# Optimization experiments

Hardware: AMD Instinct MI355X
Metric: run time of the kernel (lower is better)

The kernel has to match this reference:

```python
import jax, jax.numpy as jnp
import numpy as np

B = 262144      # batch of states (PPO rollout)
J = 16          # num_pools -> state_dim=32, action_dim=256
M = 12          # num_epochs_per_day (experts)
H = 34          # hidden_dim (fixed in source)
A = J * J


def setup_inputs() -> dict:
    key = jax.random.key(0)
    ks = jax.random.split(key, 6)
    states = jax.random.normal(ks[0], (B, 2 * J), dtype=jnp.float32)
    epoch_idx = jax.random.randint(ks[1], (B,), 0, M, dtype=jnp.int32)
    # fc1: kaiming normal (relu), zero bias
    W1 = jax.random.normal(ks[2], (H, 2 * J), dtype=jnp.float32) * np.sqrt(2.0 / (2 * J))
    b1 = jnp.zeros((H,), dtype=jnp.float32)
    # m expert output layers [M, A, H]
    Wout = jax.random.normal(ks[3], (M, A, H), dtype=jnp.float32) * np.sqrt(1.0 / H)
    bout = jax.random.normal(ks[4], (M, A), dtype=jnp.float32) * np.sqrt(1.0 / H)
    mask = jax.random.randint(ks[5], (J, J), 0, 2, dtype=jnp.int32)
    return {"states": states, "epoch_idx": epoch_idx, "W1": W1, "b1": b1,
            "Wout": Wout, "bout": bout, "mask": mask}


def reference(states, epoch_idx, W1, b1, Wout, bout, mask):
    # shared trunk: [B, H]
    x = jax.nn.relu(jnp.einsum('bs,hs->bh', states, W1) + b1)
    # grouped expert GEMM via one-hot routing (equivalent to output_layers[epoch_idx])
    onehot = jax.nn.one_hot(epoch_idx, M, dtype=x.dtype)           # [B, M]
    xe = x[:, None, :] * onehot[:, :, None]                        # [B, M, H]
    logits = jnp.einsum('bmh,mah->ba', xe, Wout) + bout[epoch_idx]  # [B, A]
    logits = logits.reshape(-1, J, J)
    NEG = jnp.float32(-1e9)
    return jnp.where(mask == 0, NEG, logits)
```

## Files before the change

### kernel.cpp

```cpp
#include <hip/hip_runtime.h>

typedef __attribute__((ext_vector_type(8))) short short8;
typedef __attribute__((ext_vector_type(4))) float f32x4;
typedef __attribute__((ext_vector_type(4))) int   i32x4;

#define SDIM 32
#define HDIM 34
#define NEXP 12
#define ACOL 256
#define SPB  256
#define MAXROWS 432
#define STG_STRIDE 260

__device__ __forceinline__ unsigned int bpack(float lo, float hi) {
    unsigned int a = __builtin_bit_cast(unsigned int, lo);
    unsigned int b = __builtin_bit_cast(unsigned int, hi);
    return ((a + 0x8000u) >> 16) | ((b + 0x8000u) & 0xffff0000u);
}

__global__ __launch_bounds__(256) void actor_kernel(
    const float* __restrict__ states,
    const int*   __restrict__ epoch_idx,
    const float* __restrict__ W1,
    const float* __restrict__ b1,
    const float* __restrict__ Wout,
    const float* __restrict__ bout,
    const int*   __restrict__ mask,
    float*       __restrict__ out,
    int nB)
{
    __shared__ unsigned int xs[MAXROWS * 32];
    __shared__ float stg[16 * STG_STRIDE];
    __shared__ unsigned short rowid[MAXROWS];
    __shared__ float w1s[HDIM * SDIM];
    __shared__ float b1s[HDIM];
    __shared__ int   cnt[NEXP];
    __shared__ int   goff[NEXP];
    __shared__ int   ntl[NEXP];

    const int t  = threadIdx.x;
    const int s0 = blockIdx.x * SPB;

    for (int i = t; i < HDIM * SDIM; i += 256) w1s[i] = W1[i];
    if (t < HDIM) b1s[t] = b1[t];
    if (t < NEXP) cnt[t] = 0;
    {
        f32x4 z = {0.f, 0.f, 0.f, 0.f};
        f32x4* xz = (f32x4*)xs;
        for (int i = t; i < MAXROWS * 8; i += 256) xz[i] = z;
        for (int i = t; i < MAXROWS; i += 256) rowid[i] = 0xFFFFu;
    }
    const int  sidx  = s0 + t;
    const bool valid = (sidx < nB);
    int e = 0, rank = 0;
    float sr[SDIM];
    if (valid) {
        const float4* sp = (const float4*)(states + (size_t)sidx * SDIM);
        #pragma unroll
        for (int q = 0; q < SDIM / 4; ++q) {
            float4 v = sp[q];
            sr[4*q+0] = v.x; sr[4*q+1] = v.y; sr[4*q+2] = v.z; sr[4*q+3] = v.w;
        }
        e = epoch_idx[sidx];
        rank = atomicAdd(&cnt[e], 1);
    }
    __syncthreads();

    if (t == 0) {
        int base = 0;
        #pragma unroll
        for (int i = 0; i < NEXP; ++i) {
            goff[i] = base;
            int nt = (cnt[i] + 15) >> 4;
            ntl[i] = nt;
            base += nt << 4;
        }
    }
    float x[HDIM];
    if (valid) {
        #pragma unroll 2
        for (int h = 0; h < HDIM; ++h) {
            float acc = b1s[h];
            const float4* wr = (const float4*)(w1s + h * SDIM);
            #pragma unroll
            for (int q = 0; q < SDIM / 4; ++q) {
                float4 wv = wr[q];
                acc = fmaf(sr[4*q+0], wv.x, acc);
                acc = fmaf(sr[4*q+1], wv.y, acc);
                acc = fmaf(sr[4*q+2], wv.z, acc);
                acc = fmaf(sr[4*q+3], wv.w, acc);
            }
            x[h] = fmaxf(acc, 0.0f);
        }
    }
    __syncthreads();

    if (valid) {
        const int slot = goff[e] + rank;
        const unsigned int swz = (unsigned int)((slot & 7) << 4);
        char* rbase = (char*)xs + slot * 128;
        unsigned int d[17];
        #pragma unroll
        for (int k = 0; k < 17; ++k) d[k] = bpack(x[2*k], x[2*k+1]);
        #pragma unroll
        for (int c = 0; c < 4; ++c) {
            f32x4 q;
            q[0] = __builtin_bit_cast(float, d[4*c+0]);
            q[1] = __builtin_bit_cast(float, d[4*c+1]);
            q[2] = __builtin_bit_cast(float, d[4*c+2]);
            q[3] = __builtin_bit_cast(float, d[4*c+3]);
            *(f32x4*)(rbase + ((unsigned)(c * 16) ^ swz)) = q;
        }
        *(unsigned int*)(rbase + (64u ^ swz)) = d[16];
        rowid[slot] = (unsigned short)t;
    }
    __syncthreads();

    const int wv   = t >> 6;
    const int lane = t & 63;
    const int r    = lane & 15;
    const int g    = lane >> 4;
    const int colbase = wv * 64 + r;
    const float NEG = -1e9f;
    const i32x4 mq = *(const i32x4*)(mask + 4 * lane);

    float* outb = out + (size_t)s0 * ACOL;

    for (int e2 = 0; e2 < NEXP; ++e2) {
        const int nt = ntl[e2];
        if (nt == 0) continue;

        short8 bf1[4], bf2[4];
        float  bias[4];
        #pragma unroll
        for (int j = 0; j < 4; ++j) {
            const int col = colbase + j * 16;
            const float* wr = Wout + ((size_t)e2 * ACOL + col) * HDIM;
            const float2* wp = (const float2*)(wr + g * 8);
            float2 p0 = wp[0], p1 = wp[1], p2 = wp[2], p3 = wp[3];
            uint4 q1 = make_uint4(bpack(p0.x, p0.y), bpack(p1.x, p1.y),
                                  bpack(p2.x, p2.y), bpack(p3.x, p3.y));
            bf1[j] = __builtin_bit_cast(short8, q1);
            uint4 q2 = make_uint4(0u, 0u, 0u, 0u);
            if (g == 0) q2.x = bpack(wr[32], wr[33]);
            bf2[j] = __builtin_bit_cast(short8, q2);
            bias[j] = bout[e2 * ACOL + col];
        }

        const int tb = goff[e2];
        for (int st = 0; st < nt; ++st) {
            const int rb  = tb + (st << 4);
            const int row = rb + r;
            const unsigned int swz = (unsigned int)((row & 7) << 4);
            const char* rp = (const char*)xs + row * 128;
            short8 a1 = *(const short8*)(rp + ((unsigned)(g * 16) ^ swz));
            short8 a2 = *(const short8*)(rp + ((unsigned)(64 + g * 16) ^ swz));

            f32x4 acc[4];
            #pragma unroll
            for (int j = 0; j < 4; ++j) {
                f32x4 a = {bias[j], bias[j], bias[j], bias[j]};
                a = __builtin_amdgcn_mfma_f32_16x16x32_bf16(a1, bf1[j], a, 0, 0, 0);
                a = __builtin_amdgcn_mfma_f32_16x16x32_bf16(a2, bf2[j], a, 0, 0, 0);
                acc[j] = a;
            }

            __syncthreads();
            #pragma unroll
            for (int j = 0; j < 4; ++j) {
                const int c = colbase + j * 16;
                #pragma unroll
                for (int i = 0; i < 4; ++i)
                    stg[(g * 4 + i) * STG_STRIDE + c] = acc[j][i];
            }
            __syncthreads();

            #pragma unroll
            for (int q = 0; q < 4; ++q) {
                const int lrow = wv * 4 + q;
                const unsigned rid = rowid[rb + lrow];
                f32x4 v = *(const f32x4*)&stg[lrow * STG_STRIDE + 4 * lane];
                v[0] = mq[0] ? v[0] : NEG;
                v[1] = mq[1] ? v[1] : NEG;
                v[2] = mq[2] ? v[2] : NEG;
                v[3] = mq[3] ? v[3] : NEG;
                if (rid != 0xFFFFu)
                    __builtin_nontemporal_store(v,
                        (f32x4*)(outb + (size_t)rid * ACOL + 4 * lane));
            }
        }
    }
}

extern "C" void kernel_launch(void* const* d_in, const int* in_sizes, int n_in,
                              void* d_out, int out_size, void* d_ws, size_t ws_size,
                              hipStream_t stream) {
    const float* states    = (const float*)d_in[0];
    const int*   epoch_idx = (const int*)  d_in[1];
    const float* W1        = (const float*)d_in[2];
    const float* b1        = (const float*)d_in[3];
    const float* Wout      = (const float*)d_in[4];
    const float* bout      = (const float*)d_in[5];
    const int*   mask      = (const int*)  d_in[6];
    float*       out       = (float*)d_out;

    const int nB   = in_sizes[0] / SDIM;
    const int grid = (nB + SPB - 1) / SPB;
    actor_kernel<<<grid, 256, 0, stream>>>(states, epoch_idx, W1, b1,
                                           Wout, bout, mask, out, nB);
}
```

Measured before the change: 98.36 us.

## Transpose MFMA output to store rows directly, removing LDS staging and barriers

Swaps the A/B operands of the MFMA so that each lane holds four consecutive output columns of one row. Lanes then write masked logits straight to global memory, with no LDS staging buffer and no two block barriers per tile. It also packs the trunk activations into 64-byte LDS rows, with the last pair kept in a separate array, and drops the zero-initialisation of the activation buffer. Masking becomes an fminf against a precomputed INF/-1e9 vector, and launch bounds request 4 blocks per CU. The trade-offs are that stores are no longer nontemporal and that masking via fminf changes NaN handling slightly.

```diff
diff --git a/kernel.cpp b/kernel.cpp
--- a/kernel.cpp
+++ b/kernel.cpp
@@ -10,7 +10,8 @@
 #define ACOL 256
 #define SPB  256
 #define MAXROWS 432
-#define STG_STRIDE 260
+#undef  MAXROWS
+#define MAXROWS 448
 
 __device__ __forceinline__ unsigned int bpack(float lo, float hi) {
     unsigned int a = __builtin_bit_cast(unsigned int, lo);
@@ -18,7 +19,7 @@
     return ((a + 0x8000u) >> 16) | ((b + 0x8000u) & 0xffff0000u);
 }
 
-__global__ __launch_bounds__(256) void actor_kernel(
+__global__ __launch_bounds__(256, 4) void actor_kernel(
     const float* __restrict__ states,
     const int*   __restrict__ epoch_idx,
     const float* __restrict__ W1,
@@ -29,14 +30,12 @@
     float*       __restrict__ out,
     int nB)
 {
-    __shared__ unsigned int xs[MAXROWS * 32];
-    __shared__ float stg[16 * STG_STRIDE];
+    __shared__ __align__(16) unsigned int xs[MAXROWS * 16];
+    __shared__ unsigned int   xt[MAXROWS];
     __shared__ unsigned short rowid[MAXROWS];
     __shared__ float w1s[HDIM * SDIM];
     __shared__ float b1s[HDIM];
-    __shared__ int   cnt[NEXP];
-    __shared__ int   goff[NEXP];
-    __shared__ int   ntl[NEXP];
+    __shared__ int   cnt[NEXP], goff[NEXP], ntl[NEXP];
 
     const int t  = threadIdx.x;
     const int s0 = blockIdx.x * SPB;
@@ -44,26 +43,25 @@
     for (int i = t; i < HDIM * SDIM; i += 256) w1s[i] = W1[i];
     if (t < HDIM) b1s[t] = b1[t];
     if (t < NEXP) cnt[t] = 0;
-    {
-        f32x4 z = {0.f, 0.f, 0.f, 0.f};
-        f32x4* xz = (f32x4*)xs;
-        for (int i = t; i < MAXROWS * 8; i += 256) xz[i] = z;
-        for (int i = t; i < MAXROWS; i += 256) rowid[i] = 0xFFFFu;
-    }
+    for (int i = t; i < MAXROWS; i += 256) rowid[i] = 0xFFFFu;
+
     const int  sidx  = s0 + t;
     const bool valid = (sidx < nB);
-    int e = 0, rank = 0;
     float sr[SDIM];
+    int e = 0;
     if (valid) {
-        const float4* sp = (const float4*)(states + (size_t)sidx * SDIM);
+        const f32x4* sp = (const f32x4*)(states + (size_t)sidx * SDIM);
         #pragma unroll
         for (int q = 0; q < SDIM / 4; ++q) {
-            float4 v = sp[q];
-            sr[4*q+0] = v.x; sr[4*q+1] = v.y; sr[4*q+2] = v.z; sr[4*q+3] = v.w;
+            f32x4 v = sp[q];
+            sr[4*q+0] = v[0]; sr[4*q+1] = v[1]; sr[4*q+2] = v[2]; sr[4*q+3] = v[3];
         }
         e = epoch_idx[sidx];
-        rank = atomicAdd(&cnt[e], 1);
-    }
+    }
+    __syncthreads();
+
+    int rank = 0;
+    if (valid) rank = atomicAdd(&cnt[e], 1);
     __syncthreads();
 
     if (t == 0) {
@@ -97,11 +95,11 @@
 
     if (valid) {
         const int slot = goff[e] + rank;
-        const unsigned int swz = (unsigned int)((slot & 7) << 4);
-        char* rbase = (char*)xs + slot * 128;
-        unsigned int d[17];
-        #pragma unroll
-        for (int k = 0; k < 17; ++k) d[k] = bpack(x[2*k], x[2*k+1]);
+        const unsigned swz = (unsigned)(slot & 3) << 4;
+        char* rbase = (char*)xs + slot * 64;
+        unsigned d[16];
+        #pragma unroll
+        for (int k = 0; k < 16; ++k) d[k] = bpack(x[2*k], x[2*k+1]);
         #pragma unroll
         for (int c = 0; c < 4; ++c) {
             f32x4 q;
@@ -109,9 +107,9 @@
             q[1] = __builtin_bit_cast(float, d[4*c+1]);
             q[2] = __builtin_bit_cast(float, d[4*c+2]);
             q[3] = __builtin_bit_cast(float, d[4*c+3]);
-            *(f32x4*)(rbase + ((unsigned)(c * 16) ^ swz)) = q;
-        }
-        *(unsigned int*)(rbase + (64u ^ swz)) = d[16];
+            *(f32x4*)(rbase + (((unsigned)(c * 16)) ^ swz)) = q;
+        }
+        xt[slot]    = bpack(x[32], x[33]);
         rowid[slot] = (unsigned short)t;
     }
     __syncthreads();
@@ -120,73 +118,74 @@
     const int lane = t & 63;
     const int r    = lane & 15;
     const int g    = lane >> 4;
-    const int colbase = wv * 64 + r;
+    const int cb0  = wv * 64 + 4 * g;
     const float NEG = -1e9f;
-    const i32x4 mq = *(const i32x4*)(mask + 4 * lane);
+    const float INF = __builtin_bit_cast(float, 0x7f800000u);
+
+    f32x4 mf[4];
+    #pragma unroll
+    for (int j = 0; j < 4; ++j) {
+        i32x4 mq = *(const i32x4*)(mask + cb0 + 16 * j);
+        mf[j][0] = mq[0] ? INF : NEG;
+        mf[j][1] = mq[1] ? INF : NEG;
+        mf[j][2] = mq[2] ? INF : NEG;
+        mf[j][3] = mq[3] ? INF : NEG;
+    }
 
     float* outb = out + (size_t)s0 * ACOL;
 
     for (int e2 = 0; e2 < NEXP; ++e2) {
-        const int nt = ntl[e2];
-        if (nt == 0) continue;
-
-        short8 bf1[4], bf2[4];
-        float  bias[4];
+        const int ntiles = ntl[e2];
+        if (ntiles == 0) continue;
+
+        short8   bf1[4];
+        unsigned w2[4];
+        f32x4    bv[4];
         #pragma unroll
         for (int j = 0; j < 4; ++j) {
-            const int col = colbase + j * 16;
+            const int col = wv * 64 + j * 16 + r;
             const float* wr = Wout + ((size_t)e2 * ACOL + col) * HDIM;
             const float2* wp = (const float2*)(wr + g * 8);
             float2 p0 = wp[0], p1 = wp[1], p2 = wp[2], p3 = wp[3];
             uint4 q1 = make_uint4(bpack(p0.x, p0.y), bpack(p1.x, p1.y),
                                   bpack(p2.x, p2.y), bpack(p3.x, p3.y));
             bf1[j] = __builtin_bit_cast(short8, q1);
-            uint4 q2 = make_uint4(0u, 0u, 0u, 0u);
-            if (g == 0) q2.x = bpack(wr[32], wr[33]);
-            bf2[j] = __builtin_bit_cast(short8, q2);
-            bias[j] = bout[e2 * ACOL + col];
+            w2[j]  = (g == 0) ? bpack(wr[32], wr[33]) : 0u;
+            bv[j]  = *(const f32x4*)(bout + e2 * ACOL + cb0 + 16 * j);
         }
 
         const int tb = goff[e2];
-        for (int st = 0; st < nt; ++st) {
-            const int rb  = tb + (st << 4);
-            const int row = rb + r;
-            const unsigned int swz = (unsigned int)((row & 7) << 4);
-            const char* rp = (const char*)xs + row * 128;
-            short8 a1 = *(const short8*)(rp + ((unsigned)(g * 16) ^ swz));
-            short8 a2 = *(const short8*)(rp + ((unsigned)(64 + g * 16) ^ swz));
+        for (int st = 0; st < ntiles; ++st) {
+            const int row = tb + (st << 4) + r;
+            const char* rp = (const char*)xs + row * 64;
+            short8 a1 = *(const short8*)(rp + (((unsigned)(g * 16)) ^ ((unsigned)(row & 3) << 4)));
+            const unsigned xtv = xt[row];
+            const unsigned rid = rowid[row];
+            short8 a2 = __builtin_bit_cast(short8,
+                          make_uint4(g == 0 ? xtv : 0u, 0u, 0u, 0u));
 
             f32x4 acc[4];
             #pragma unroll
             for (int j = 0; j < 4; ++j) {
-                f32x4 a = {bias[j], bias[j], bias[j], bias[j]};
-                a = __builtin_amdgcn_mfma_f32_16x16x32_bf16(a1, bf1[j], a, 0, 0, 0);
-                a = __builtin_amdgcn_mfma_f32_16x16x32_bf16(a2, bf2[j], a, 0, 0, 0);
+                f32x4 a = bv[j];
+                a = __builtin_amdgcn_mfma_f32_16x16x32_bf16(bf1[j], a1, a, 0, 0, 0);
+                short8 b2 = __builtin_bit_cast(short8,
+                              make_uint4(w2[j], 0u, 0u, 0u));
+                a = __builtin_amdgcn_mfma_f32_16x16x32_bf16(b2, a2, a, 0, 0, 0);
                 acc[j] = a;
             }
 
-            __syncthreads();
-            #pragma unroll
-            for (int j = 0; j < 4; ++j) {
-                const int c = colbase + j * 16;
+            if (rid != 0xFFFFu) {
+                float* ob = outb + (size_t)rid * ACOL + cb0;
                 #pragma unroll
-                for (int i = 0; i < 4; ++i)
-                    stg[(g * 4 + i) * STG_STRIDE + c] = acc[j][i];
-            }
-            __syncthreads();
-
-            #pragma unroll
-            for (int q = 0; q < 4; ++q) {
-                const int lrow = wv * 4 + q;
-                const unsigned rid = rowid[rb + lrow];
-                f32x4 v = *(const f32x4*)&stg[lrow * STG_STRIDE + 4 * lane];
-                v[0] = mq[0] ? v[0] : NEG;
-                v[1] = mq[1] ? v[1] : NEG;
-                v[2] = mq[2] ? v[2] : NEG;
-                v[3] = mq[3] ? v[3] : NEG;
-                if (rid != 0xFFFFu)
-                    __builtin_nontemporal_store(v,
-                        (f32x4*)(outb + (size_t)rid * ACOL + 4 * lane));
+                for (int j = 0; j < 4; ++j) {
+                    f32x4 v = acc[j];
+                    v[0] = fminf(v[0], mf[j][0]);
+                    v[1] = fminf(v[1], mf[j][1]);
+                    v[2] = fminf(v[2], mf[j][2]);
+                    v[3] = fminf(v[3], mf[j][3]);
+                    *(f32x4*)(ob + 16 * j) = v;
+                }
             }
         }
     }
```

Result: slower. 103.6 us (+5.3%).
